# Performance work log

Measured on AMD Instinct MI355X. Metric: run time of the kernel, lower is better.

## Reference

```python
import jax, jax.numpy as jnp
import numpy as np

B, T, C, H = 1, 1024, 2048, 32
N = C // H  # head_dim = 64
EPS_GN = 0.00064


def setup_inputs() -> dict:
    key = jax.random.key(0)
    ks = jax.random.split(key, 40)
    f32 = jnp.float32

    def rn(k, shape, s):
        return jax.random.normal(k, shape, f32) * s

    layer_idx, n_layer = 12, 24
    r01 = layer_idx / (n_layer - 1)
    r1a0 = 1.0 - layer_idx / n_layer
    ddd = (jnp.arange(C, dtype=f32) / C).reshape(1, 1, C)
    decay_speed = -7.0 + 5.0 * (jnp.arange(C, dtype=f32) / (C - 1)) ** (0.85 + r01 ** 0.5)

    inp = dict(
        hidden_states=jax.random.normal(ks[0], (B, T, C), f32),
        Wq=rn(ks[1], (C, C), 0.02), Wk=rn(ks[2], (C, C), 0.02),
        Wv=rn(ks[3], (C, C), 0.02), Wo=rn(ks[4], (C, C), 0.02),
        time_maa_x=1.0 - ddd ** (0.6 * r1a0 ** 0.9),
        time_maa_rg=rn(ks[5], (1, 1, C), 0.01),
        time_maa_wa=rn(ks[6], (1, 1, C), 0.01),
        time_maa_k=rn(ks[7], (1, 1, C), 0.01),
        time_maa_v=rn(ks[8], (1, 1, C), 0.01),
        time_maa_w1=rn(ks[9], (C, 4 * 32), 0.01),
        time_maa_w2=rn(ks[10], (4, 32, C), 0.01),
        time_decay=decay_speed.reshape(1, 1, C) + 0.5,
        time_decay_w1=rn(ks[11], (C, 64), 0.01),
        time_decay_w2=rn(ks[12], (64, C), 0.01),
        time_aaaaa=rn(ks[13], (1, 1, C), 0.01),
        time_aaa_w1=rn(ks[14], (C, 16), 0.01),
        time_aaa_w2=rn(ks[15], (16, C), 0.01),
        time_kkk_w1=rn(ks[16], (C, 16), 0.01),
        time_kkk_w2=rn(ks[17], (16, C), 0.01),
        gate_w1=rn(ks[18], (C, 128), 0.01),
        gate_w2=rn(ks[19], (128, C), 0.01),
        time_misc_a=rn(ks[20], (1, 1, C), 0.01),
        ma_w1=rn(ks[21], (C, 16), 0.01),
        ma_w2=rn(ks[22], (16, C), 0.01),
        time_misc_k=rn(ks[23], (1, 1, C), 0.01),
        mk_w1=rn(ks[24], (C, 16), 0.01),
        mk_w2=rn(ks[25], (16, C), 0.01),
        time_faaaa=rn(ks[26], (1, 1, H, N), 0.01),
        ln_w=1.0 + rn(ks[27], (C,), 0.01),
        ln_b=rn(ks[28], (C,), 0.01),
    )
    return inp


def _wkv7(r, w, k, v, a, b):
    """RWKV7 matrix-state recurrence. Inputs [B,T,C]; per head state [N,N].
    state_t = state * exp(w_t) (per key-col) + (state @ a_t) b_t^T + v_t k_t^T;
    out_t = state_t @ r_t."""
    hs = lambda x: x.reshape(B, T, H, N)
    r, k, v, a, b = map(hs, (r, k, v, a, b))
    dec = jnp.exp(hs(w))  # w <= -0.5, decay in (0,1)

    def step(state, inp):
        r_t, d_t, k_t, v_t, a_t, b_t = inp  # each [B,H,N]
        sa = jnp.einsum('bhij,bhj->bhi', state, a_t)
        state = (state * d_t[:, :, None, :]
                 + sa[..., None] * b_t[:, :, None, :]
                 + v_t[..., None] * k_t[:, :, None, :])
        out = jnp.einsum('bhij,bhj->bhi', state, r_t)
        return state, out

    xs = tuple(jnp.moveaxis(t, 1, 0) for t in (r, dec, k, v, a, b))  # [T,B,H,N]
    state0 = jnp.zeros((B, H, N, N), r.dtype)
    _, out = jax.lax.scan(step, state0, xs)
    return jnp.moveaxis(out, 0, 1).reshape(B, T, C)


def _group_norm(x, w, b):
    xg = x.reshape(B, T, H, N)
    mu = xg.mean(-1, keepdims=True)
    var = xg.var(-1, keepdims=True)
    xn = (xg - mu) * jax.lax.rsqrt(var + EPS_GN)
    return xn.reshape(B, T, C) * w + b


def reference(hidden_states, Wq, Wk, Wv, Wo, time_maa_x, time_maa_rg, time_maa_wa,
              time_maa_k, time_maa_v, time_maa_w1, time_maa_w2, time_decay,
              time_decay_w1, time_decay_w2, time_aaaaa, time_aaa_w1, time_aaa_w2,
              time_kkk_w1, time_kkk_w2, gate_w1, gate_w2, time_misc_a, ma_w1, ma_w2,
              time_misc_k, mk_w1, mk_w2, time_faaaa, ln_w, ln_b):
    x = hidden_states  # T already multiple of 16, so no padding branch
    dxprev = jnp.pad(x, ((0, 0), (1, 0), (0, 0)))[:, :-1] - x  # token shift
    xxx = x + dxprev * time_maa_x
    mix = jnp.tanh(xxx @ time_maa_w1).reshape(B, T, 4, 32)
    mix = jnp.einsum('btfd,fdc->fbtc', mix, time_maa_w2)  # [4,B,T,C]
    mrg, mwa, mk_mix, mv = mix[0], mix[1], mix[2], mix[3]
    xrg = x + dxprev * (time_maa_rg + mrg)
    xwa = x + dxprev * (time_maa_wa + mwa)
    xk = x + dxprev * (time_maa_k + mk_mix)
    xv = x + dxprev * (time_maa_v + mv)

    r = xrg @ Wq
    w = -jax.nn.softplus(-(time_decay + jnp.tanh(xwa @ time_decay_w1) @ time_decay_w2)) - 0.5
    k = xk @ Wk
    v = xv @ Wv
    g = jnp.tanh(xrg @ gate_w1) @ gate_w2

    kk = k + jnp.tanh(xk @ time_kkk_w1) @ time_kkk_w2
    kkh = kk.reshape(B, T, H, N)
    kk = (kkh / jnp.maximum(jnp.linalg.norm(kkh, axis=-1, keepdims=True), 1e-12)).reshape(B, T, C)

    a = jax.nn.sigmoid(time_aaaaa + (xwa @ time_aaa_w1) @ time_aaa_w2)
    ma = jax.nn.sigmoid(time_misc_a + (xwa @ ma_w1) @ ma_w2)
    k = k * ma + k * a * (1.0 - ma)
    mk_g = jax.nn.sigmoid(time_misc_k + (xk @ mk_w1) @ mk_w2)
    k = k * jnp.exp(jnp.minimum(w * mk_g, 0.0))

    y = _wkv7(r, w, k, v, -kk, kk * a)
    y = _group_norm(y, ln_w, ln_b)
    rh, kh, vh = (t.reshape(B, T, H, N) for t in (r, k, v))
    y = y + ((rh * kh * time_faaaa).sum(-1, keepdims=True) * vh).reshape(B, T, C)
    return (y * g) @ Wo
```

## Files before the change

kernel.cpp:

```cpp
#include <hip/hip_runtime.h>


#define T_ 1024
#define C_ 2048
#define H_ 32
#define N_ 64

using half8  = __attribute__((ext_vector_type(8))) _Float16;
using half4  = __attribute__((ext_vector_type(4))) _Float16;
using floatx4 = __attribute__((ext_vector_type(4))) float;

#define DPP_ADD(v, ctrl) \
    ((v) + __int_as_float(__builtin_amdgcn_update_dpp( \
        0, __float_as_int(v), (ctrl), 0xf, 0xf, true)))
#define REDUCE16(v) do { \
    v = DPP_ADD(v, 0xB1); v = DPP_ADD(v, 0x4E); \
    v = DPP_ADD(v, 0x141); v = DPP_ADD(v, 0x140); } while (0)

__device__ __forceinline__ void async_cp16(const void* g, void* l) {
    __builtin_amdgcn_global_load_lds(
        (const __attribute__((address_space(1))) void*)g,
        (__attribute__((address_space(3))) void*)l, 16, 0, 0);
}

__global__ __launch_bounds__(256) void k_tr(
    const float* __restrict__ W0, const float* __restrict__ W1,
    const float* __restrict__ W2, const float* __restrict__ W3,
    _Float16* __restrict__ D0, _Float16* __restrict__ D1,
    _Float16* __restrict__ D2, _Float16* __restrict__ D3)
{
    const int z = blockIdx.z;
    const float* S = (z == 0) ? W0 : (z == 1) ? W1 : (z == 2) ? W2 : W3;
    _Float16* D = (z == 0) ? D0 : (z == 1) ? D1 : (z == 2) ? D2 : D3;
    const int nb = blockIdx.x * 64, kb = blockIdx.y * 64;
    __shared__ __align__(16) float tile[64][65];
    const int tr = threadIdx.x >> 4, tc4 = (threadIdx.x & 15) * 4;
#pragma unroll
    for (int p = 0; p < 4; ++p) {
        int row = p * 16 + tr;
        float4 v = *(const float4*)&S[(size_t)(kb + row) * C_ + nb + tc4];
        tile[row][tc4 + 0] = v.x; tile[row][tc4 + 1] = v.y;
        tile[row][tc4 + 2] = v.z; tile[row][tc4 + 3] = v.w;
    }
    __syncthreads();
#pragma unroll
    for (int p = 0; p < 4; ++p) {
        int n = p * 16 + tr;
        half4 u;
        u[0] = (_Float16)tile[tc4 + 0][n];
        u[1] = (_Float16)tile[tc4 + 1][n];
        u[2] = (_Float16)tile[tc4 + 2][n];
        u[3] = (_Float16)tile[tc4 + 3][n];
        *(half4*)&D[(size_t)(nb + n) * C_ + kb + tc4] = u;
    }
}

__global__ __launch_bounds__(256) void k_trW(
    const float* __restrict__ maa_w1, const float* __restrict__ gate_w1,
    const float* __restrict__ decay_w1, const float* __restrict__ aaa_w1,
    const float* __restrict__ ma_w1, const float* __restrict__ kkk_w1,
    const float* __restrict__ mk_w1,
    _Float16* __restrict__ WTm, _Float16* __restrict__ WTl)
{
    const int z = blockIdx.z;
    const int k = blockIdx.x * 256 + threadIdx.x;
    const int n = blockIdx.y;
    if (z == 0 && n >= 128) return;
    const float* src; int stride, col;
    _Float16* dst;
    if (z == 0) { src = maa_w1; stride = 128; col = n; dst = WTm; }
    else {
        dst = WTl;
        if (n < 128)      { src = gate_w1;  stride = 128; col = n; }
        else if (n < 192) { src = decay_w1; stride = 64;  col = n - 128; }
        else if (n < 208) { src = aaa_w1;   stride = 16;  col = n - 192; }
        else if (n < 224) { src = ma_w1;    stride = 16;  col = n - 208; }
        else if (n < 240) { src = kkk_w1;   stride = 16;  col = n - 224; }
        else              { src = mk_w1;    stride = 16;  col = n - 240; }
    }
    dst[(size_t)n * C_ + k] = (_Float16)src[(size_t)k * stride + col];
}

__global__ __launch_bounds__(256) void k_prep(
    const float* __restrict__ X, const float* __restrict__ maa_x,
    _Float16* __restrict__ xxxH)
{
    const size_t idx = (size_t)blockIdx.x * 256 + threadIdx.x;
    const int c = (int)(idx & (C_ - 1));
    float cur = X[idx];
    float prev = (idx >= C_) ? X[idx - C_] : 0.0f;
    xxxH[idx] = (_Float16)(cur + (prev - cur) * maa_x[c]);
}

__global__ __launch_bounds__(256) void k_lora(
    int which,
    const _Float16* __restrict__ Axxx, const _Float16* __restrict__ Axrg,
    const _Float16* __restrict__ Axwa, const _Float16* __restrict__ Axk,
    const _Float16* __restrict__ WTm, const _Float16* __restrict__ WTl,
    float* __restrict__ m1p, float* __restrict__ l2p)
{
    const int mt = blockIdx.x;
    const int nt = blockIdx.y;
    const int ks = blockIdx.z;
    const _Float16* A; const _Float16* BT; float* O; int ostride;
    if (which == 0) { A = Axxx; BT = WTm; O = m1p; ostride = 128; }
    else {
        BT = WTl; O = l2p; ostride = 256;
        A = (nt < 4) ? Axrg : (nt < 7) ? Axwa : Axk;
    }
    O += (size_t)ks * T_ * ostride;
    const int m0 = mt * 64, n0 = nt * 32, k0 = ks * 512;
    const int tid = threadIdx.x;
    __shared__ __align__(16) _Float16 As[64 * 40];
    __shared__ __align__(16) _Float16 Bs[32 * 40];
    const int lane = tid & 63, wv = tid >> 6;
    const int r16 = lane & 15, q = lane >> 4;

    floatx4 acc[2];
    { floatx4 zv = {0.f, 0.f, 0.f, 0.f}; acc[0] = zv; acc[1] = zv; }

    const int arow = tid >> 2, ac8 = (tid & 3) * 8;
    const _Float16* ag = A + (size_t)(m0 + arow) * C_ + k0 + ac8;
    const _Float16* bg = BT + (size_t)(n0 + (tid >> 2)) * C_ + k0 + ac8;

    for (int kc = 0; kc < 512; kc += 32) {
        half8 av = *(const half8*)(ag + kc);
        half8 bv;
        if (tid < 128) bv = *(const half8*)(bg + kc);
        *(half8*)&As[arow * 40 + ac8] = av;
        if (tid < 128) *(half8*)&Bs[(tid >> 2) * 40 + ac8] = bv;
        __syncthreads();
        half8 af = *(const half8*)&As[(wv * 16 + r16) * 40 + q * 8];
        half8 b0 = *(const half8*)&Bs[(r16) * 40 + q * 8];
        half8 b1 = *(const half8*)&Bs[(16 + r16) * 40 + q * 8];
        acc[0] = __builtin_amdgcn_mfma_f32_16x16x32_f16(af, b0, acc[0], 0, 0, 0);
        acc[1] = __builtin_amdgcn_mfma_f32_16x16x32_f16(af, b1, acc[1], 0, 0, 0);
        __syncthreads();
    }
#pragma unroll
    for (int j = 0; j < 2; ++j)
#pragma unroll
        for (int e = 0; e < 4; ++e) {
            int row = m0 + wv * 16 + q * 4 + e;
            int col = n0 + j * 16 + r16;
            O[(size_t)row * ostride + col] = acc[j][e];
        }
}

__global__ __launch_bounds__(256) void k_xmix(
    const float* __restrict__ X, const float* __restrict__ m1p,
    const float* __restrict__ w2,
    const float* __restrict__ mrg, const float* __restrict__ mwa,
    const float* __restrict__ mk, const float* __restrict__ mv,
    _Float16* __restrict__ xrgH, _Float16* __restrict__ xwaH,
    _Float16* __restrict__ xkH, _Float16* __restrict__ xvH)
{
    const int tid = threadIdx.x;
    const int c = blockIdx.x * 256 + tid;
    const int t0 = blockIdx.y * 16;
    const size_t P = (size_t)T_ * 128;
    __shared__ __align__(16) float m1s[16][128];
#pragma unroll
    for (int p = 0; p < 2; ++p) {
        int id = tid + p * 256;
        int r = id >> 5, c4 = (id & 31) * 4;
        size_t off = (size_t)(t0 + r) * 128 + c4;
        float4 v0 = *(const float4*)&m1p[off];
        float4 v1 = *(const float4*)&m1p[P + off];
        float4 v2 = *(const float4*)&m1p[2 * P + off];
        float4 v3 = *(const float4*)&m1p[3 * P + off];
        float4 v;
        v.x = tanhf(((v0.x + v1.x) + v2.x) + v3.x);
        v.y = tanhf(((v0.y + v1.y) + v2.y) + v3.y);
        v.z = tanhf(((v0.z + v1.z) + v2.z) + v3.z);
        v.w = tanhf(((v0.w + v1.w) + v2.w) + v3.w);
        *(float4*)&m1s[r][c4] = v;
    }
    __syncthreads();
    float a0[16], a1[16], a2[16], a3[16];
#pragma unroll
    for (int t = 0; t < 16; ++t) { a0[t] = 0.f; a1[t] = 0.f; a2[t] = 0.f; a3[t] = 0.f; }
    for (int d = 0; d < 32; ++d) {
        float w0 = w2[(size_t)(0 * 32 + d) * C_ + c];
        float w1 = w2[(size_t)(1 * 32 + d) * C_ + c];
        float w2v = w2[(size_t)(2 * 32 + d) * C_ + c];
        float w3 = w2[(size_t)(3 * 32 + d) * C_ + c];
#pragma unroll
        for (int t = 0; t < 16; ++t) {
            a0[t] = fmaf(m1s[t][d],      w0,  a0[t]);
            a1[t] = fmaf(m1s[t][32 + d], w1,  a1[t]);
            a2[t] = fmaf(m1s[t][64 + d], w2v, a2[t]);
            a3[t] = fmaf(m1s[t][96 + d], w3,  a3[t]);
        }
    }
    float vrg = mrg[c], vwa = mwa[c], vmk = mk[c], vmv = mv[c];
    float prev = (t0 > 0) ? X[(size_t)(t0 - 1) * C_ + c] : 0.0f;
    for (int t = 0; t < 16; ++t) {
        size_t idx = (size_t)(t0 + t) * C_ + c;
        float cur = X[idx];
        float dx = prev - cur;
        xrgH[idx] = (_Float16)(cur + dx * (vrg + a0[t]));
        xwaH[idx] = (_Float16)(cur + dx * (vwa + a1[t]));
        xkH[idx]  = (_Float16)(cur + dx * (vmk + a2[t]));
        xvH[idx]  = (_Float16)(cur + dx * (vmv + a3[t]));
        prev = cur;
    }
}

__global__ __launch_bounds__(256) void k_gemm(
    const _Float16* __restrict__ A0, const _Float16* __restrict__ B0, float* __restrict__ C0,
    const _Float16* __restrict__ A1, const _Float16* __restrict__ B1, float* __restrict__ C1,
    const _Float16* __restrict__ A2, const _Float16* __restrict__ B2, float* __restrict__ C2)
{
    const int z = blockIdx.z;
    const _Float16* A = (z == 0) ? A0 : (z == 1) ? A1 : A2;
    const _Float16* Bt = (z == 0) ? B0 : (z == 1) ? B1 : B2;
    float* C = (z == 0) ? C0 : (z == 1) ? C1 : C2;
    const int mtile = blockIdx.y * 128;
    const int ntile = blockIdx.x * 128;
    const int tid = threadIdx.x;
    __shared__ __align__(16) _Float16 As[3][128 * 32];
    __shared__ __align__(16) _Float16 Bs[3][128 * 32];
    const int lane = tid & 63;
    const int wvid = tid >> 6;
    const int wm = wvid >> 1, wn = wvid & 1;
    const int r16 = lane & 15, q = lane >> 4;
    const int qs = (q ^ ((r16 >> 1) & 3)) * 8;

    floatx4 acc[4][4];
#pragma unroll
    for (int i = 0; i < 4; ++i)
#pragma unroll
        for (int j = 0; j < 4; ++j) { floatx4 zv = {0.f, 0.f, 0.f, 0.f}; acc[i][j] = zv; }

    const int srow = tid >> 2, sq = tid & 3;
    const int sqg = (sq ^ ((srow >> 1) & 3)) * 8;
    const _Float16* agA = A + (size_t)(mtile + srow) * C_ + sqg;
    const _Float16* agB = Bt + (size_t)(ntile + srow) * C_ + sqg;
    const int ldso = srow * 32 + sq * 8;
    const size_t rowoff = (size_t)64 * C_;

#define G_STAGE(pb, koff) do {                                                \
        async_cp16(agA + (koff), &As[pb][ldso]);                              \
        async_cp16(agA + (koff) + rowoff, &As[pb][ldso + 64 * 32]);           \
        async_cp16(agB + (koff), &Bs[pb][ldso]);                              \
        async_cp16(agB + (koff) + rowoff, &Bs[pb][ldso + 64 * 32]);           \
    } while (0)

    G_STAGE(0, 0);
    G_STAGE(1, 32);
    __builtin_amdgcn_sched_barrier(0);
    asm volatile("s_waitcnt vmcnt(4)" ::: "memory");
    __builtin_amdgcn_s_barrier();
    __builtin_amdgcn_sched_barrier(0);

    for (int ks = 0; ks < 64; ++ks) {
        const int p = ks % 3;
        if (ks + 2 < 64) G_STAGE((ks + 2) % 3, (ks + 2) * 32);
        half8 af[4], bf[4];
#pragma unroll
        for (int i = 0; i < 4; ++i)
            af[i] = *(const half8*)&As[p][(wm * 64 + i * 16 + r16) * 32 + qs];
#pragma unroll
        for (int j = 0; j < 4; ++j)
            bf[j] = *(const half8*)&Bs[p][(wn * 64 + j * 16 + r16) * 32 + qs];
#pragma unroll
        for (int i = 0; i < 4; ++i)
#pragma unroll
            for (int j = 0; j < 4; ++j)
                acc[i][j] = __builtin_amdgcn_mfma_f32_16x16x32_f16(af[i], bf[j], acc[i][j], 0, 0, 0);
        __builtin_amdgcn_sched_barrier(0);
        if (ks + 2 < 64)
            asm volatile("s_waitcnt vmcnt(4)" ::: "memory");
        else
            asm volatile("s_waitcnt vmcnt(0)" ::: "memory");
        __builtin_amdgcn_s_barrier();
        __builtin_amdgcn_sched_barrier(0);
    }
#pragma unroll
    for (int i = 0; i < 4; ++i)
#pragma unroll
        for (int j = 0; j < 4; ++j)
#pragma unroll
            for (int e = 0; e < 4; ++e) {
                int row = mtile + wm * 64 + i * 16 + q * 4 + e;
                int col = ntile + wn * 64 + j * 16 + r16;
                C[(size_t)row * C_ + col] = acc[i][j][e];
            }
#undef G_STAGE
}

__global__ __launch_bounds__(256) void k_gemm64(
    const _Float16* __restrict__ A0, const _Float16* __restrict__ B0, float* __restrict__ C0)
{
    const _Float16* A = A0;
    const _Float16* Bt = B0;
    float* C = C0;
    const int mtile = blockIdx.y * 128;
    const int ntile = blockIdx.x * 64;
    const int tid = threadIdx.x;
    __shared__ __align__(16) _Float16 As[3][128 * 32];
    __shared__ __align__(16) _Float16 Bs[3][64 * 32];
    const int lane = tid & 63;
    const int wvid = tid >> 6;
    const int wm = wvid >> 1, wn = wvid & 1;
    const int r16 = lane & 15, q = lane >> 4;
    const int qs = (q ^ ((r16 >> 1) & 3)) * 8;

    floatx4 acc[4][2];
#pragma unroll
    for (int i = 0; i < 4; ++i)
#pragma unroll
        for (int j = 0; j < 2; ++j) { floatx4 zv = {0.f, 0.f, 0.f, 0.f}; acc[i][j] = zv; }

    const int srow = tid >> 2, sq = tid & 3;
    const int sqg = (sq ^ ((srow >> 1) & 3)) * 8;
    const _Float16* agA = A + (size_t)(mtile + srow) * C_ + sqg;
    const _Float16* agB = Bt + (size_t)(ntile + srow) * C_ + sqg;
    const int ldso = srow * 32 + sq * 8;
    const size_t rowoff = (size_t)64 * C_;

#define G_STAGE(pb, koff) do {                                                \
        async_cp16(agA + (koff), &As[pb][ldso]);                              \
        async_cp16(agA + (koff) + rowoff, &As[pb][ldso + 64 * 32]);           \
        async_cp16(agB + (koff), &Bs[pb][ldso]);                              \
    } while (0)

    G_STAGE(0, 0);
    G_STAGE(1, 32);
    __builtin_amdgcn_sched_barrier(0);
    asm volatile("s_waitcnt vmcnt(3)" ::: "memory");
    __builtin_amdgcn_s_barrier();
    __builtin_amdgcn_sched_barrier(0);

    for (int ks = 0; ks < 64; ++ks) {
        const int p = ks % 3;
        if (ks + 2 < 64) G_STAGE((ks + 2) % 3, (ks + 2) * 32);
        half8 af[4], bf[2];
#pragma unroll
        for (int i = 0; i < 4; ++i)
            af[i] = *(const half8*)&As[p][(wm * 64 + i * 16 + r16) * 32 + qs];
#pragma unroll
        for (int j = 0; j < 2; ++j)
            bf[j] = *(const half8*)&Bs[p][(wn * 32 + j * 16 + r16) * 32 + qs];
#pragma unroll
        for (int i = 0; i < 4; ++i)
#pragma unroll
            for (int j = 0; j < 2; ++j)
                acc[i][j] = __builtin_amdgcn_mfma_f32_16x16x32_f16(af[i], bf[j], acc[i][j], 0, 0, 0);
        __builtin_amdgcn_sched_barrier(0);
        if (ks + 2 < 64)
            asm volatile("s_waitcnt vmcnt(3)" ::: "memory");
        else
            asm volatile("s_waitcnt vmcnt(0)" ::: "memory");
        __builtin_amdgcn_s_barrier();
        __builtin_amdgcn_sched_barrier(0);
    }
#pragma unroll
    for (int i = 0; i < 4; ++i)
#pragma unroll
        for (int j = 0; j < 2; ++j)
#pragma unroll
            for (int e = 0; e < 4; ++e) {
                int row = mtile + wm * 64 + i * 16 + q * 4 + e;
                int col = ntile + wn * 32 + j * 16 + r16;
                C[(size_t)row * C_ + col] = acc[i][j][e];
            }
#undef G_STAGE
}

__global__ __launch_bounds__(256) void k_fuse(
    const float* __restrict__ l2p,
    float* __restrict__ K0,
    const float* __restrict__ decay_w2, const float* __restrict__ aaa_w2,
    const float* __restrict__ ma_w2, const float* __restrict__ kkk_w2,
    const float* __restrict__ mk_w2,
    const float* __restrict__ tdecay, const float* __restrict__ aaaaa,
    const float* __restrict__ misc_a, const float* __restrict__ misc_k,
    float* __restrict__ Dout, float* __restrict__ KKout, float* __restrict__ Bout)
{
    const int tid = threadIdx.x;
    const int c = blockIdx.x * 256 + tid;
    const int t0 = blockIdx.y * 4;
    const size_t P = (size_t)T_ * 256;
    __shared__ __align__(16) float wsS[4][96];
    __shared__ __align__(16) float ksS[4][32];
    if (tid < 4 * 24) {
        int r = tid / 24, c4 = (tid % 24) * 4;
        size_t off = (size_t)(t0 + r) * 256 + 128 + c4;
        float4 v0 = *(const float4*)&l2p[off];
        float4 v1 = *(const float4*)&l2p[P + off];
        float4 v2 = *(const float4*)&l2p[2 * P + off];
        float4 v3 = *(const float4*)&l2p[3 * P + off];
        float4 v;
        v.x = ((v0.x + v1.x) + v2.x) + v3.x;
        v.y = ((v0.y + v1.y) + v2.y) + v3.y;
        v.z = ((v0.z + v1.z) + v2.z) + v3.z;
        v.w = ((v0.w + v1.w) + v2.w) + v3.w;
        if (c4 < 64) { v.x = tanhf(v.x); v.y = tanhf(v.y); v.z = tanhf(v.z); v.w = tanhf(v.w); }
        *(float4*)&wsS[r][c4] = v;
    }
    if (tid < 4 * 8) {
        int r = tid / 8, c4 = (tid % 8) * 4;
        size_t off = (size_t)(t0 + r) * 256 + 224 + c4;
        float4 v0 = *(const float4*)&l2p[off];
        float4 v1 = *(const float4*)&l2p[P + off];
        float4 v2 = *(const float4*)&l2p[2 * P + off];
        float4 v3 = *(const float4*)&l2p[3 * P + off];
        float4 v;
        v.x = ((v0.x + v1.x) + v2.x) + v3.x;
        v.y = ((v0.y + v1.y) + v2.y) + v3.y;
        v.z = ((v0.z + v1.z) + v2.z) + v3.z;
        v.w = ((v0.w + v1.w) + v2.w) + v3.w;
        if (c4 < 16) { v.x = tanhf(v.x); v.y = tanhf(v.y); v.z = tanhf(v.z); v.w = tanhf(v.w); }
        *(float4*)&ksS[r][c4] = v;
    }
    __syncthreads();
    float accW[4], accA[4], accMA[4], accKK[4], accMK[4];
#pragma unroll
    for (int r = 0; r < 4; ++r) { accW[r] = 0.f; accA[r] = 0.f; accMA[r] = 0.f; accKK[r] = 0.f; accMK[r] = 0.f; }
    for (int j = 0; j < 64; ++j) {
        float w = decay_w2[(size_t)j * C_ + c];
#pragma unroll
        for (int r = 0; r < 4; ++r) accW[r] = fmaf(wsS[r][j], w, accW[r]);
    }
    for (int j = 0; j < 16; ++j) {
        float wa = aaa_w2[(size_t)j * C_ + c];
        float wm = ma_w2[(size_t)j * C_ + c];
        float wk = kkk_w2[(size_t)j * C_ + c];
        float wq = mk_w2[(size_t)j * C_ + c];
#pragma unroll
        for (int r = 0; r < 4; ++r) {
            accA[r]  = fmaf(wsS[r][64 + j], wa, accA[r]);
            accMA[r] = fmaf(wsS[r][80 + j], wm, accMA[r]);
            accKK[r] = fmaf(ksS[r][j],      wk, accKK[r]);
            accMK[r] = fmaf(ksS[r][16 + j], wq, accMK[r]);
        }
    }
    float td = tdecay[c], aa = aaaaa[c], mia = misc_a[c], mik = misc_k[c];
#pragma unroll
    for (int r = 0; r < 4; ++r) {
        size_t idx = (size_t)(t0 + r) * C_ + c;
        float wraw = td + accW[r];
        float w = -__logf(1.0f + __expf(-wraw)) - 0.5f;
        float a  = 1.0f / (1.0f + __expf(-(aa  + accA[r])));
        float mav = 1.0f / (1.0f + __expf(-(mia + accMA[r])));
        float mkv = 1.0f / (1.0f + __expf(-(mik + accMK[r])));
        float k0 = K0[idx];
        float kkun = k0 + accKK[r];
        float ss = kkun * kkun;
        REDUCE16(ss);
        ss += __shfl_xor(ss, 16, 64);
        ss += __shfl_xor(ss, 32, 64);
        float kn = kkun * (1.0f / fmaxf(sqrtf(ss), 1e-12f));
        Dout[idx]  = __expf(w);
        KKout[idx] = kn;
        Bout[idx]  = kn * a;
        K0[idx]    = k0 * (mav + a * (1.0f - mav)) * __expf(fminf(w * mkv, 0.0f));
    }
}

__global__ __launch_bounds__(512) void k_wkv_p1(
    const float* __restrict__ DEC, const float* __restrict__ K,
    const float* __restrict__ V, const float* __restrict__ KK,
    const float* __restrict__ Bb,
    float* __restrict__ Send, float* __restrict__ Pend)
{
    const int tid = threadIdx.x;
    const int g = blockIdx.x;
    const int h = blockIdx.y;
    const int c0 = h * 64;
    const int wv = tid >> 6, lane = tid & 63;
    const int jg = lane & 15, q = lane >> 4, j4 = jg * 4;
    const bool isS = wv < 4;
    const int row0 = (isS ? wv : wv - 4) * 16 + q * 4;

    __shared__ __align__(16) float dS[2][16][64], kS[2][16][64], vS[2][16][64],
                                   aS[2][16][64], bS[2][16][64];

    const int pos = tid & 255, grp = tid >> 8;
    const int pst = pos >> 4, pq4 = (pos & 15) * 4;

#define P1_STAGE(buf, tcb) do {                                               \
    size_t gg = (size_t)((tcb) + pst) * C_ + c0 + pq4;                        \
    if (grp == 0) { async_cp16(&DEC[gg], &dS[buf][pst][pq4]);                 \
                    async_cp16(&KK[gg],  &aS[buf][pst][pq4]);                 \
                    async_cp16(&Bb[gg],  &bS[buf][pst][pq4]); }               \
    else          { async_cp16(&K[gg], &kS[buf][pst][pq4]);                   \
                    async_cp16(&V[gg], &vS[buf][pst][pq4]); }                 \
} while (0)

    float4 s0, s1, s2, s3;
    if (isS) {
        s0 = make_float4(0.f, 0.f, 0.f, 0.f); s1 = s0; s2 = s0; s3 = s0;
    } else {
#define IDROW(m) make_float4((j4 + 0 == row0 + (m)) ? 1.f : 0.f,              \
                             (j4 + 1 == row0 + (m)) ? 1.f : 0.f,              \
                             (j4 + 2 == row0 + (m)) ? 1.f : 0.f,              \
                             (j4 + 3 == row0 + (m)) ? 1.f : 0.f)
        s0 = IDROW(0); s1 = IDROW(1); s2 = IDROW(2); s3 = IDROW(3);
#undef IDROW
    }

    const int t0 = g * 128;
    P1_STAGE(0, t0);

    for (int tc = 0; tc < 128; tc += 16) {
        const int p = (tc >> 4) & 1;
        __syncthreads();
        if (tc + 16 < 128) P1_STAGE(p ^ 1, t0 + tc + 16);
#pragma unroll
        for (int tt = 0; tt < 16; ++tt) {
            float4 cd = *(float4*)&dS[p][tt][j4];
            float4 ca = *(float4*)&aS[p][tt][j4];
            float4 cb = *(float4*)&bS[p][tt][j4];
            float4 ck, vv;
            if (isS) {
                ck = *(float4*)&kS[p][tt][j4];
                vv = *(float4*)&vS[p][tt][row0];
            } else {
                ck = make_float4(0.f, 0.f, 0.f, 0.f);
                vv = make_float4(0.f, 0.f, 0.f, 0.f);
            }
            float sa0 = -(fmaf(s0.y, ca.y, s0.x * ca.x) + fmaf(s0.w, ca.w, s0.z * ca.z));
            float sa1 = -(fmaf(s1.y, ca.y, s1.x * ca.x) + fmaf(s1.w, ca.w, s1.z * ca.z));
            float sa2 = -(fmaf(s2.y, ca.y, s2.x * ca.x) + fmaf(s2.w, ca.w, s2.z * ca.z));
            float sa3 = -(fmaf(s3.y, ca.y, s3.x * ca.x) + fmaf(s3.w, ca.w, s3.z * ca.z));
            REDUCE16(sa0); REDUCE16(sa1); REDUCE16(sa2); REDUCE16(sa3);
            s0.x = fmaf(s0.x, cd.x, fmaf(sa0, cb.x, vv.x * ck.x));
            s0.y = fmaf(s0.y, cd.y, fmaf(sa0, cb.y, vv.x * ck.y));
            s0.z = fmaf(s0.z, cd.z, fmaf(sa0, cb.z, vv.x * ck.z));
            s0.w = fmaf(s0.w, cd.w, fmaf(sa0, cb.w, vv.x * ck.w));
            s1.x = fmaf(s1.x, cd.x, fmaf(sa1, cb.x, vv.y * ck.x));
            s1.y = fmaf(s1.y, cd.y, fmaf(sa1, cb.y, vv.y * ck.y));
            s1.z = fmaf(s1.z, cd.z, fmaf(sa1, cb.z, vv.y * ck.z));
            s1.w = fmaf(s1.w, cd.w, fmaf(sa1, cb.w, vv.y * ck.w));
            s2.x = fmaf(s2.x, cd.x, fmaf(sa2, cb.x, vv.z * ck.x));
            s2.y = fmaf(s2.y, cd.y, fmaf(sa2, cb.y, vv.z * ck.y));
            s2.z = fmaf(s2.z, cd.z, fmaf(sa2, cb.z, vv.z * ck.z));
            s2.w = fmaf(s2.w, cd.w, fmaf(sa2, cb.w, vv.z * ck.w));
            s3.x = fmaf(s3.x, cd.x, fmaf(sa3, cb.x, vv.w * ck.x));
            s3.y = fmaf(s3.y, cd.y, fmaf(sa3, cb.y, vv.w * ck.y));
            s3.z = fmaf(s3.z, cd.z, fmaf(sa3, cb.z, vv.w * ck.z));
            s3.w = fmaf(s3.w, cd.w, fmaf(sa3, cb.w, vv.w * ck.w));
        }
    }
    float* dst = isS ? Send : Pend;
    size_t base = (size_t)((h * 7 + g) * 64 + row0) * 64 + j4;
    *(float4*)&dst[base +   0] = s0;
    *(float4*)&dst[base +  64] = s1;
    *(float4*)&dst[base + 128] = s2;
    *(float4*)&dst[base + 192] = s3;
#undef P1_STAGE
}

__global__ __launch_bounds__(256) void k_wkv_comb(
    const float* __restrict__ Send, const float* __restrict__ Pend,
    float* __restrict__ Sin)
{
    const int h = blockIdx.x;
    const int tid = threadIdx.x;
    const int i = tid >> 2;
    const int jq = (tid & 3) * 16;
    __shared__ float Sc[64][65];
    __shared__ __align__(16) float Pl[64][64];

    float4 z4 = make_float4(0.f, 0.f, 0.f, 0.f);
#pragma unroll
    for (int c = 0; c < 16; c += 4)
        *(float4*)&Sin[(size_t)(h * 8) * 4096 + (size_t)i * 64 + jq + c] = z4;
#pragma unroll
    for (int c = 0; c < 16; ++c) Sc[i][jq + c] = 0.f;
    __syncthreads();

    for (int g = 1; g < 8; ++g) {
        const float* Pg = &Pend[(size_t)(h * 7 + g - 1) * 4096];
        for (int idx = tid * 4; idx < 4096; idx += 1024) {
            float4 v = *(const float4*)&Pg[idx];
            *(float4*)&Pl[idx >> 6][idx & 63] = v;
        }
        __syncthreads();
        float acc[16];
        const float* Sg = &Send[(size_t)(h * 7 + g - 1) * 4096 + (size_t)i * 64 + jq];
#pragma unroll
        for (int c = 0; c < 16; c += 4) {
            float4 v = *(const float4*)&Sg[c];
            acc[c] = v.x; acc[c + 1] = v.y; acc[c + 2] = v.z; acc[c + 3] = v.w;
        }
        for (int k = 0; k < 64; ++k) {
            float sik = Sc[i][k];
#pragma unroll
            for (int c = 0; c < 16; ++c) acc[c] = fmaf(sik, Pl[k][jq + c], acc[c]);
        }
        __syncthreads();
        float* So = &Sin[(size_t)(h * 8 + g) * 4096 + (size_t)i * 64 + jq];
#pragma unroll
        for (int c = 0; c < 16; ++c) Sc[i][jq + c] = acc[c];
#pragma unroll
        for (int c = 0; c < 16; c += 4) {
            float4 v = make_float4(acc[c], acc[c + 1], acc[c + 2], acc[c + 3]);
            *(float4*)&So[c] = v;
        }
        __syncthreads();
    }
}

__global__ __launch_bounds__(256) void k_wkv_p2(
    const float* __restrict__ R, const float* __restrict__ DEC,
    const float* __restrict__ K, const float* __restrict__ V,
    const float* __restrict__ KK, const float* __restrict__ Bb,
    const float* __restrict__ Sin, float* __restrict__ Y)
{
    const int tid = threadIdx.x;
    const int g = blockIdx.x;
    const int h = blockIdx.y;
    const int c0 = h * 64;
    const int wv = tid >> 6, lane = tid & 63;
    const int jg = lane & 15, q = lane >> 4, j4 = jg * 4;
    const int row0 = wv * 16 + q * 4;

    __shared__ __align__(16) float rS[2][16][64], dS[2][16][64], kS[2][16][64],
                                   aS[2][16][64], bS[2][16][64], vS[2][16][64];

    const int pst = tid >> 4, pq4 = (tid & 15) * 4;

#define P2_STAGE(buf, tcb) do {                                               \
    size_t gg = (size_t)((tcb) + pst) * C_ + c0 + pq4;                        \
    async_cp16(&R[gg],   &rS[buf][pst][pq4]);                                 \
    async_cp16(&DEC[gg], &dS[buf][pst][pq4]);                                 \
    async_cp16(&K[gg],   &kS[buf][pst][pq4]);                                 \
    async_cp16(&V[gg],   &vS[buf][pst][pq4]);                                 \
    async_cp16(&KK[gg],  &aS[buf][pst][pq4]);                                 \
    async_cp16(&Bb[gg],  &bS[buf][pst][pq4]);                                 \
} while (0)

    float4 s0, s1, s2, s3;
    {
        const float* Sb = &Sin[(size_t)((h * 8 + g) * 64 + row0) * 64 + j4];
        s0 = *(const float4*)&Sb[0];
        s1 = *(const float4*)&Sb[64];
        s2 = *(const float4*)&Sb[128];
        s3 = *(const float4*)&Sb[192];
    }

    const int t0 = g * 128;
    P2_STAGE(0, t0);

    for (int tc = 0; tc < 128; tc += 16) {
        const int p = (tc >> 4) & 1;
        __syncthreads();
        if (tc + 16 < 128) P2_STAGE(p ^ 1, t0 + tc + 16);
#pragma unroll
        for (int hh = 0; hh < 2; ++hh) {
            float po0[8], po1[8], po2[8], po3[8];
#pragma unroll
            for (int qs2 = 0; qs2 < 8; ++qs2) {
                const int tt = hh * 8 + qs2;
                float4 cr = *(float4*)&rS[p][tt][j4];
                float4 cd = *(float4*)&dS[p][tt][j4];
                float4 ck = *(float4*)&kS[p][tt][j4];
                float4 ca = *(float4*)&aS[p][tt][j4];
                float4 cb = *(float4*)&bS[p][tt][j4];
                float4 vv = *(float4*)&vS[p][tt][row0];
                float sa0 = -(fmaf(s0.y, ca.y, s0.x * ca.x) + fmaf(s0.w, ca.w, s0.z * ca.z));
                float sa1 = -(fmaf(s1.y, ca.y, s1.x * ca.x) + fmaf(s1.w, ca.w, s1.z * ca.z));
                float sa2 = -(fmaf(s2.y, ca.y, s2.x * ca.x) + fmaf(s2.w, ca.w, s2.z * ca.z));
                float sa3 = -(fmaf(s3.y, ca.y, s3.x * ca.x) + fmaf(s3.w, ca.w, s3.z * ca.z));
                REDUCE16(sa0); REDUCE16(sa1); REDUCE16(sa2); REDUCE16(sa3);
                s0.x = fmaf(s0.x, cd.x, fmaf(sa0, cb.x, vv.x * ck.x));
                s0.y = fmaf(s0.y, cd.y, fmaf(sa0, cb.y, vv.x * ck.y));
                s0.z = fmaf(s0.z, cd.z, fmaf(sa0, cb.z, vv.x * ck.z));
                s0.w = fmaf(s0.w, cd.w, fmaf(sa0, cb.w, vv.x * ck.w));
                s1.x = fmaf(s1.x, cd.x, fmaf(sa1, cb.x, vv.y * ck.x));
                s1.y = fmaf(s1.y, cd.y, fmaf(sa1, cb.y, vv.y * ck.y));
                s1.z = fmaf(s1.z, cd.z, fmaf(sa1, cb.z, vv.y * ck.z));
                s1.w = fmaf(s1.w, cd.w, fmaf(sa1, cb.w, vv.y * ck.w));
                s2.x = fmaf(s2.x, cd.x, fmaf(sa2, cb.x, vv.z * ck.x));
                s2.y = fmaf(s2.y, cd.y, fmaf(sa2, cb.y, vv.z * ck.y));
                s2.z = fmaf(s2.z, cd.z, fmaf(sa2, cb.z, vv.z * ck.z));
                s2.w = fmaf(s2.w, cd.w, fmaf(sa2, cb.w, vv.z * ck.w));
                s3.x = fmaf(s3.x, cd.x, fmaf(sa3, cb.x, vv.w * ck.x));
                s3.y = fmaf(s3.y, cd.y, fmaf(sa3, cb.y, vv.w * ck.y));
                s3.z = fmaf(s3.z, cd.z, fmaf(sa3, cb.z, vv.w * ck.z));
                s3.w = fmaf(s3.w, cd.w, fmaf(sa3, cb.w, vv.w * ck.w));
                po0[qs2] = fmaf(s0.w, cr.w, fmaf(s0.z, cr.z, fmaf(s0.y, cr.y, s0.x * cr.x)));
                po1[qs2] = fmaf(s1.w, cr.w, fmaf(s1.z, cr.z, fmaf(s1.y, cr.y, s1.x * cr.x)));
                po2[qs2] = fmaf(s2.w, cr.w, fmaf(s2.z, cr.z, fmaf(s2.y, cr.y, s2.x * cr.x)));
                po3[qs2] = fmaf(s3.w, cr.w, fmaf(s3.z, cr.z, fmaf(s3.y, cr.y, s3.x * cr.x)));
            }
#pragma unroll
            for (int qs2 = 0; qs2 < 8; ++qs2) {
                REDUCE16(po0[qs2]); REDUCE16(po1[qs2]);
                REDUCE16(po2[qs2]); REDUCE16(po3[qs2]);
            }
            if (jg == 0) {
#pragma unroll
                for (int qs2 = 0; qs2 < 8; ++qs2) {
                    float4 o = make_float4(po0[qs2], po1[qs2], po2[qs2], po3[qs2]);
                    *(float4*)&Y[(size_t)(t0 + tc + hh * 8 + qs2) * C_ + c0 + row0] = o;
                }
            }
        }
    }
#undef P2_STAGE
}

__global__ __launch_bounds__(256) void k_gn(
    const float* __restrict__ Y, const float* __restrict__ R, const float* __restrict__ K,
    const float* __restrict__ V, const float* __restrict__ l2p,
    const float* __restrict__ gw2,
    const float* __restrict__ faaaa, const float* __restrict__ lnw,
    const float* __restrict__ lnb, _Float16* __restrict__ YG)
{
    const int tid = threadIdx.x;
    const int c = blockIdx.x * 256 + tid;
    const int t0 = blockIdx.y * 16;
    const size_t P = (size_t)T_ * 256;
    __shared__ __align__(16) float gs[16][128];
    for (int id = tid; id < 16 * 128; id += 256) {
        int r = id >> 7, cc = id & 127;
        size_t off = (size_t)(t0 + r) * 256 + cc;
        float v = ((l2p[off] + l2p[P + off]) + l2p[2 * P + off]) + l2p[3 * P + off];
        gs[r][cc] = tanhf(v);
    }
    __syncthreads();
    float gacc[16];
#pragma unroll
    for (int r = 0; r < 16; ++r) gacc[r] = 0.f;
    for (int j = 0; j < 128; ++j) {
        float w = gw2[(size_t)j * C_ + c];
#pragma unroll
        for (int r = 0; r < 16; ++r) gacc[r] = fmaf(gs[r][j], w, gacc[r]);
    }
    float fa = faaaa[c], lw = lnw[c], lb = lnb[c];
    for (int r = 0; r < 16; ++r) {
        const size_t idx = (size_t)(t0 + r) * C_ + c;
        float y = Y[idx];
        float s1 = y, s2 = y * y;
#pragma unroll
        for (int off = 1; off < 64; off <<= 1) {
            s1 += __shfl_xor(s1, off, 64);
            s2 += __shfl_xor(s2, off, 64);
        }
        float mu = s1 * (1.0f / 64.0f);
        float var = s2 * (1.0f / 64.0f) - mu * mu;
        float gn = (y - mu) * rsqrtf(var + 0.00064f) * lw + lb;
        float p = R[idx] * K[idx] * fa;
#pragma unroll
        for (int off = 1; off < 64; off <<= 1) p += __shfl_xor(p, off, 64);
        float y2 = gn + p * V[idx];
        YG[idx] = (_Float16)(y2 * gacc[r]);
    }
}

extern "C" void kernel_launch(void* const* d_in, const int* in_sizes, int n_in,
                              void* d_out, int out_size, void* d_ws, size_t ws_size,
                              hipStream_t stream)
{
    (void)in_sizes; (void)n_in; (void)out_size; (void)ws_size;
    const float* hidden   = (const float*)d_in[0];
    const float* Wq       = (const float*)d_in[1];
    const float* Wk       = (const float*)d_in[2];
    const float* Wv       = (const float*)d_in[3];
    const float* Wo       = (const float*)d_in[4];
    const float* maa_x    = (const float*)d_in[5];
    const float* maa_rg   = (const float*)d_in[6];
    const float* maa_wa   = (const float*)d_in[7];
    const float* maa_k    = (const float*)d_in[8];
    const float* maa_v    = (const float*)d_in[9];
    const float* maa_w1   = (const float*)d_in[10];
    const float* maa_w2   = (const float*)d_in[11];
    const float* tdecay   = (const float*)d_in[12];
    const float* decay_w1 = (const float*)d_in[13];
    const float* decay_w2 = (const float*)d_in[14];
    const float* aaaaa    = (const float*)d_in[15];
    const float* aaa_w1   = (const float*)d_in[16];
    const float* aaa_w2   = (const float*)d_in[17];
    const float* kkk_w1   = (const float*)d_in[18];
    const float* kkk_w2   = (const float*)d_in[19];
    const float* gate_w1  = (const float*)d_in[20];
    const float* gate_w2  = (const float*)d_in[21];
    const float* misc_a   = (const float*)d_in[22];
    const float* ma_w1    = (const float*)d_in[23];
    const float* ma_w2    = (const float*)d_in[24];
    const float* misc_k   = (const float*)d_in[25];
    const float* mk_w1    = (const float*)d_in[26];
    const float* mk_w2    = (const float*)d_in[27];
    const float* faaaa    = (const float*)d_in[28];
    const float* lnw      = (const float*)d_in[29];
    const float* lnb      = (const float*)d_in[30];

    float* ws = (float*)d_ws;
    const size_t TC = (size_t)T_ * C_;
    float* S0 = ws + 0 * TC;
    float* Send = ws + 1 * TC;
    float* Pend = Send + (size_t)32 * 7 * 64 * 64;
    float* S2 = ws + 2 * TC;
    float* S3 = ws + 3 * TC;
    float* S4 = ws + 4 * TC;
    float* S5 = ws + 5 * TC;
    float* S6 = ws + 6 * TC;
    float* S7 = ws + 7 * TC;
    float* m1p = ws + 8 * TC;
    float* l2p = m1p + (size_t)4 * T_ * 128;
    _Float16* WTq = (_Float16*)(l2p + (size_t)4 * T_ * 256);
    _Float16* WTk = WTq + (size_t)C_ * C_;
    _Float16* WTv = WTk + (size_t)C_ * C_;
    _Float16* WTo = WTv + (size_t)C_ * C_;
    _Float16* WTm = WTo + (size_t)C_ * C_;
    _Float16* WTl = WTm + (size_t)128 * C_;
    _Float16* xxxH = WTl + (size_t)256 * C_;
    _Float16* xrgH = xxxH + TC;
    _Float16* xwaH = xrgH + TC;
    _Float16* xkH  = xwaH + TC;
    _Float16* xvH  = xkH + TC;
    _Float16* ygH  = xxxH;
    float* Sin = (float*)xrgH;
    float* out = (float*)d_out;

    k_tr<<<dim3(32, 32, 4), 256, 0, stream>>>(Wq, Wk, Wv, Wo, WTq, WTk, WTv, WTo);
    k_trW<<<dim3(8, 256, 2), 256, 0, stream>>>(maa_w1, gate_w1, decay_w1,
        aaa_w1, ma_w1, kkk_w1, mk_w1, WTm, WTl);
    k_prep<<<dim3((int)(TC / 256)), 256, 0, stream>>>(hidden, maa_x, xxxH);
    k_lora<<<dim3(16, 4, 4), 256, 0, stream>>>(0, xxxH, xxxH, xxxH, xxxH,
        WTm, WTl, m1p, l2p);
    k_xmix<<<dim3(8, 64), 256, 0, stream>>>(hidden, m1p, maa_w2,
        maa_rg, maa_wa, maa_k, maa_v, xrgH, xwaH, xkH, xvH);
    k_lora<<<dim3(16, 8, 4), 256, 0, stream>>>(1, xxxH, xrgH, xwaH, xkH,
        WTm, WTl, m1p, l2p);
    k_gemm<<<dim3(16, 8, 3), 256, 0, stream>>>(
        xrgH, WTq, S4,  xkH, WTk, S6,  xvH, WTv, S7);
    k_fuse<<<dim3(8, 256), 256, 0, stream>>>(l2p, S6, decay_w2, aaa_w2, ma_w2,
        kkk_w2, mk_w2, tdecay, aaaaa, misc_a, misc_k, S5, S3, S2);
    k_wkv_p1<<<dim3(7, 32), 512, 0, stream>>>(S5, S6, S7, S3, S2, Send, Pend);
    k_wkv_comb<<<dim3(32), 256, 0, stream>>>(Send, Pend, Sin);
    k_wkv_p2<<<dim3(8, 32), 256, 0, stream>>>(S4, S5, S6, S7, S3, S2, Sin, S0);
    k_gn<<<dim3(8, 64), 256, 0, stream>>>(S0, S4, S6, S7, l2p, gate_w2,
        faaaa, lnw, lnb, ygH);
    k_gemm64<<<dim3(32, 8, 1), 256, 0, stream>>>(ygH, WTo, out);
}
```

Before: 522.4 us.

## Split WKV7 time chunks from 128 to 64 steps for more parallel blocks

Halves the WKV chunk length, so phase 1 runs 15 chunks per head and phase 2 runs 16, roughly doubling the number of blocks and shortening each block's serial recurrence. The combine kernel now uses 1024 threads and chains 15 chunk transitions instead of 7. Pend moves into the fp16 activation region to fit the larger buffers. The cost is a longer serial combine chain and twice as much chunk-state traffic.

```diff
diff --git a/kernel.cpp b/kernel.cpp
--- a/kernel.cpp
+++ b/kernel.cpp
@@ -502,13 +502,13 @@
 #undef IDROW
     }
 
-    const int t0 = g * 128;
+    const int t0 = g * 64;
     P1_STAGE(0, t0);
 
-    for (int tc = 0; tc < 128; tc += 16) {
+    for (int tc = 0; tc < 64; tc += 16) {
         const int p = (tc >> 4) & 1;
         __syncthreads();
-        if (tc + 16 < 128) P1_STAGE(p ^ 1, t0 + tc + 16);
+        if (tc + 16 < 64) P1_STAGE(p ^ 1, t0 + tc + 16);
 #pragma unroll
         for (int tt = 0; tt < 16; ++tt) {
             float4 cd = *(float4*)&dS[p][tt][j4];
@@ -546,7 +546,7 @@
         }
     }
     float* dst = isS ? Send : Pend;
-    size_t base = (size_t)((h * 7 + g) * 64 + row0) * 64 + j4;
+    size_t base = (size_t)((h * 15 + g) * 64 + row0) * 64 + j4;
     *(float4*)&dst[base +   0] = s0;
     *(float4*)&dst[base +  64] = s1;
     *(float4*)&dst[base + 128] = s2;
@@ -554,53 +554,47 @@
 #undef P1_STAGE
 }
 
-__global__ __launch_bounds__(256) void k_wkv_comb(
+__global__ __launch_bounds__(1024) void k_wkv_comb(
     const float* __restrict__ Send, const float* __restrict__ Pend,
     float* __restrict__ Sin)
 {
     const int h = blockIdx.x;
     const int tid = threadIdx.x;
-    const int i = tid >> 2;
-    const int jq = (tid & 3) * 16;
+    const int i = tid >> 4;
+    const int jq = (tid & 15) * 4;
     __shared__ float Sc[64][65];
     __shared__ __align__(16) float Pl[64][64];
 
     float4 z4 = make_float4(0.f, 0.f, 0.f, 0.f);
-#pragma unroll
-    for (int c = 0; c < 16; c += 4)
-        *(float4*)&Sin[(size_t)(h * 8) * 4096 + (size_t)i * 64 + jq + c] = z4;
-#pragma unroll
-    for (int c = 0; c < 16; ++c) Sc[i][jq + c] = 0.f;
+    *(float4*)&Sin[(size_t)(h * 16) * 4096 + (size_t)i * 64 + jq] = z4;
+    Sc[i][jq + 0] = 0.f; Sc[i][jq + 1] = 0.f;
+    Sc[i][jq + 2] = 0.f; Sc[i][jq + 3] = 0.f;
     __syncthreads();
 
-    for (int g = 1; g < 8; ++g) {
-        const float* Pg = &Pend[(size_t)(h * 7 + g - 1) * 4096];
-        for (int idx = tid * 4; idx < 4096; idx += 1024) {
+    for (int g = 1; g < 16; ++g) {
+        const float* Pg = &Pend[(size_t)(h * 15 + g - 1) * 4096];
+        {
+            int idx = tid * 4;
             float4 v = *(const float4*)&Pg[idx];
             *(float4*)&Pl[idx >> 6][idx & 63] = v;
         }
         __syncthreads();
-        float acc[16];
-        const float* Sg = &Send[(size_t)(h * 7 + g - 1) * 4096 + (size_t)i * 64 + jq];
-#pragma unroll
-        for (int c = 0; c < 16; c += 4) {
-            float4 v = *(const float4*)&Sg[c];
-            acc[c] = v.x; acc[c + 1] = v.y; acc[c + 2] = v.z; acc[c + 3] = v.w;
+        float acc[4];
+        {
+            float4 sv = *(const float4*)&Send[
+                (size_t)(h * 15 + g - 1) * 4096 + (size_t)i * 64 + jq];
+            acc[0] = sv.x; acc[1] = sv.y; acc[2] = sv.z; acc[3] = sv.w;
         }
         for (int k = 0; k < 64; ++k) {
             float sik = Sc[i][k];
 #pragma unroll
-            for (int c = 0; c < 16; ++c) acc[c] = fmaf(sik, Pl[k][jq + c], acc[c]);
+            for (int c = 0; c < 4; ++c) acc[c] = fmaf(sik, Pl[k][jq + c], acc[c]);
         }
         __syncthreads();
-        float* So = &Sin[(size_t)(h * 8 + g) * 4096 + (size_t)i * 64 + jq];
-#pragma unroll
-        for (int c = 0; c < 16; ++c) Sc[i][jq + c] = acc[c];
-#pragma unroll
-        for (int c = 0; c < 16; c += 4) {
-            float4 v = make_float4(acc[c], acc[c + 1], acc[c + 2], acc[c + 3]);
-            *(float4*)&So[c] = v;
-        }
+        float* So = &Sin[(size_t)(h * 16 + g) * 4096 + (size_t)i * 64 + jq];
+        Sc[i][jq + 0] = acc[0]; Sc[i][jq + 1] = acc[1];
+        Sc[i][jq + 2] = acc[2]; Sc[i][jq + 3] = acc[3];
+        *(float4*)So = make_float4(acc[0], acc[1], acc[2], acc[3]);
         __syncthreads();
     }
 }
@@ -636,20 +630,20 @@
 
     float4 s0, s1, s2, s3;
     {
-        const float* Sb = &Sin[(size_t)((h * 8 + g) * 64 + row0) * 64 + j4];
+        const float* Sb = &Sin[(size_t)((h * 16 + g) * 64 + row0) * 64 + j4];
         s0 = *(const float4*)&Sb[0];
         s1 = *(const float4*)&Sb[64];
         s2 = *(const float4*)&Sb[128];
         s3 = *(const float4*)&Sb[192];
     }
 
-    const int t0 = g * 128;
+    const int t0 = g * 64;
     P2_STAGE(0, t0);
 
-    for (int tc = 0; tc < 128; tc += 16) {
+    for (int tc = 0; tc < 64; tc += 16) {
         const int p = (tc >> 4) & 1;
         __syncthreads();
-        if (tc + 16 < 128) P2_STAGE(p ^ 1, t0 + tc + 16);
+        if (tc + 16 < 64) P2_STAGE(p ^ 1, t0 + tc + 16);
 #pragma unroll
         for (int hh = 0; hh < 2; ++hh) {
             float po0[8], po1[8], po2[8], po3[8];
@@ -794,7 +788,6 @@
     const size_t TC = (size_t)T_ * C_;
     float* S0 = ws + 0 * TC;
     float* Send = ws + 1 * TC;
-    float* Pend = Send + (size_t)32 * 7 * 64 * 64;
     float* S2 = ws + 2 * TC;
     float* S3 = ws + 3 * TC;
     float* S4 = ws + 4 * TC;
@@ -815,7 +808,8 @@
     _Float16* xkH  = xwaH + TC;
     _Float16* xvH  = xkH + TC;
     _Float16* ygH  = xxxH;
-    float* Sin = (float*)xrgH;
+    float* Sin  = (float*)xrgH;
+    float* Pend = (float*)xkH;
     float* out = (float*)d_out;
 
     k_tr<<<dim3(32, 32, 4), 256, 0, stream>>>(Wq, Wk, Wv, Wo, WTq, WTk, WTv, WTo);
@@ -832,9 +826,9 @@
         xrgH, WTq, S4,  xkH, WTk, S6,  xvH, WTv, S7);
     k_fuse<<<dim3(8, 256), 256, 0, stream>>>(l2p, S6, decay_w2, aaa_w2, ma_w2,
         kkk_w2, mk_w2, tdecay, aaaaa, misc_a, misc_k, S5, S3, S2);
-    k_wkv_p1<<<dim3(7, 32), 512, 0, stream>>>(S5, S6, S7, S3, S2, Send, Pend);
-    k_wkv_comb<<<dim3(32), 256, 0, stream>>>(Send, Pend, Sin);
-    k_wkv_p2<<<dim3(8, 32), 256, 0, stream>>>(S4, S5, S6, S7, S3, S2, Sin, S0);
+    k_wkv_p1<<<dim3(15, 32), 512, 0, stream>>>(S5, S6, S7, S3, S2, Send, Pend);
+    k_wkv_comb<<<dim3(32), 1024, 0, stream>>>(Send, Pend, Sin);
+    k_wkv_p2<<<dim3(16, 32), 256, 0, stream>>>(S4, S5, S6, S7, S3, S2, Sin, S0);
     k_gn<<<dim3(8, 64), 256, 0, stream>>>(S0, S4, S6, S7, l2p, gate_w2,
         faaaa, lnw, lnb, ygH);
     k_gemm64<<<dim3(32, 8, 1), 256, 0, stream>>>(ygH, WTo, out);
```

Result: no change. 524.0 us (+0.3%).
